# Kernel optimization log

Hardware: AMD Instinct MI355X
Metric: run time of the kernel (lower is better)

## Reference

```python
import jax, jax.numpy as jnp
import numpy as np

EPS = 1e-8
HIDDEN = 200


def _dsmall(n, d):
    # torch: d = d*(d>eps) + eps*(d<=eps); n/d
    return n / jnp.where(d > EPS, d, EPS)


def _mp_match(v1, v2, w):
    # v1: (B,S,H); v2: (B,S,H) or (B,H); w: (L,H) -> (B,S,L)
    wt = w.T[None, None]                      # (1,1,H,L)
    a = v1[..., None] * wt                    # (B,S,H,L)
    if v2.ndim == 2:
        v2 = jnp.broadcast_to(v2[:, None, :], v1.shape)
    b = v2[..., None] * wt                    # (B,S,H,L)
    dot = jnp.sum(a * b, axis=2)
    na = jnp.linalg.norm(a, axis=2)
    nb = jnp.linalg.norm(b, axis=2)
    return dot / jnp.maximum(na * nb, EPS)    # cosine_similarity over H


def _mp_pairwise(v1, v2, w):
    # v1: (B,S1,H); v2: (B,S2,H); w: (L,H) -> (B,S1,S2,L)
    a = v1[:, None] * w[None, :, None]        # (B,L,S1,H)
    b = v2[:, None] * w[None, :, None]        # (B,L,S2,H)
    na = jnp.linalg.norm(a, axis=3, keepdims=True)   # (B,L,S1,1)
    nb = jnp.linalg.norm(b, axis=3, keepdims=True)   # (B,L,S2,1)
    n = jnp.einsum('blph,blqh->blpq', a, b)
    d = na * jnp.swapaxes(nb, 2, 3)
    return jnp.transpose(_dsmall(n, d), (0, 2, 3, 1))


def _attention(v1, v2):
    # cosine-similarity matrix (B,S1,S2)
    n1 = jnp.linalg.norm(v1, axis=2, keepdims=True)           # (B,S1,1)
    n2 = jnp.linalg.norm(v2, axis=2, keepdims=True)           # (B,S2,1)
    a = jnp.einsum('bph,bqh->bpq', v1, v2)
    return _dsmall(a, n1 * jnp.swapaxes(n2, 1, 2))


def _matching(con_p, con_h, w1, w2, w3, w4, w5, w6, w7, w8):
    p_fw, p_bw = con_p[..., :HIDDEN], con_p[..., HIDDEN:]
    h_fw, h_bw = con_h[..., :HIDDEN], con_h[..., HIDDEN:]

    # 1) full matching
    mv_p_full_fw = _mp_match(p_fw, h_fw[:, -1, :], w1)
    mv_p_full_bw = _mp_match(p_bw, h_bw[:, 0, :], w2)
    mv_h_full_fw = _mp_match(h_fw, p_fw[:, -1, :], w1)
    mv_h_full_bw = _mp_match(h_bw, p_bw[:, 0, :], w2)

    # 2) maxpooling matching
    mv_max_fw = _mp_pairwise(p_fw, h_fw, w3)  # (B,S1,S2,L)
    mv_max_bw = _mp_pairwise(p_bw, h_bw, w4)
    mv_p_max_fw = jnp.max(mv_max_fw, axis=2)
    mv_p_max_bw = jnp.max(mv_max_bw, axis=2)
    mv_h_max_fw = jnp.max(mv_max_fw, axis=1)
    mv_h_max_bw = jnp.max(mv_max_bw, axis=1)

    # 3) attentive matching (mean)
    att_fw = _attention(p_fw, h_fw)           # (B,S1,S2)
    att_bw = _attention(p_bw, h_bw)

    # sum of att_h over dim 2 is a matmul (same math, no (B,S1,S2,H) tensor)
    att_h_sum_fw = jnp.einsum('bpq,bqh->bph', att_fw, h_fw)
    att_h_sum_bw = jnp.einsum('bpq,bqh->bph', att_bw, h_bw)
    att_p_sum_fw = jnp.einsum('bpq,bph->bqh', att_fw, p_fw)
    att_p_sum_bw = jnp.einsum('bpq,bph->bqh', att_bw, p_bw)

    att_mean_h_fw = _dsmall(att_h_sum_fw, jnp.sum(att_fw, axis=2, keepdims=True))
    att_mean_h_bw = _dsmall(att_h_sum_bw, jnp.sum(att_bw, axis=2, keepdims=True))
    att_mean_p_fw = _dsmall(att_p_sum_fw, jnp.swapaxes(jnp.sum(att_fw, axis=1, keepdims=True), 1, 2))
    att_mean_p_bw = _dsmall(att_p_sum_bw, jnp.swapaxes(jnp.sum(att_bw, axis=1, keepdims=True), 1, 2))

    mv_p_att_mean_fw = _mp_match(p_fw, att_mean_h_fw, w5)
    mv_p_att_mean_bw = _mp_match(p_bw, att_mean_h_bw, w6)
    mv_h_att_mean_fw = _mp_match(h_fw, att_mean_p_fw, w5)
    mv_h_att_mean_bw = _mp_match(h_bw, att_mean_p_bw, w6)

    # 4) max-attentive matching (needs full (B,S1,S2,H) broadcast for the max)
    att_h_fw = h_fw[:, None, :, :] * att_fw[:, :, :, None]   # (B,S1,S2,H)
    att_h_bw = h_bw[:, None, :, :] * att_bw[:, :, :, None]
    att_p_fw = p_fw[:, :, None, :] * att_fw[:, :, :, None]
    att_p_bw = p_bw[:, :, None, :] * att_bw[:, :, :, None]

    att_max_h_fw = jnp.max(att_h_fw, axis=2)                 # (B,S1,H)
    att_max_h_bw = jnp.max(att_h_bw, axis=2)
    att_max_p_fw = jnp.max(att_p_fw, axis=1)                 # (B,S2,H)
    att_max_p_bw = jnp.max(att_p_bw, axis=1)

    mv_p_att_max_fw = _mp_match(p_fw, att_max_h_fw, w7)
    mv_p_att_max_bw = _mp_match(p_bw, att_max_h_bw, w8)
    mv_h_att_max_fw = _mp_match(h_fw, att_max_p_fw, w7)
    mv_h_att_max_bw = _mp_match(h_bw, att_max_p_bw, w8)

    mv_p = jnp.concatenate([mv_p_full_fw, mv_p_max_fw, mv_p_att_mean_fw, mv_p_att_max_fw,
                            mv_p_full_bw, mv_p_max_bw, mv_p_att_mean_bw, mv_p_att_max_bw], axis=2)
    mv_h = jnp.concatenate([mv_h_full_fw, mv_h_max_fw, mv_h_att_mean_fw, mv_h_att_max_fw,
                            mv_h_full_bw, mv_h_max_bw, mv_h_att_mean_bw, mv_h_att_max_bw], axis=2)
    # dropout is identity in inference mode
    return mv_p, mv_h


def setup_inputs() -> dict:
    key = jax.random.key(0)
    ks = jax.random.split(key, 10)
    B, S, H, L = 32, 64, HIDDEN, 20
    w_std = np.sqrt(2.0 / H)  # kaiming_normal fan_in
    inp = {
        'con_p': jax.random.normal(ks[0], (B, S, 2 * H), dtype=jnp.float32),
        'con_h': jax.random.normal(ks[1], (B, S, 2 * H), dtype=jnp.float32),
    }
    for i in range(8):
        inp[f'mp_w{i+1}'] = jax.random.normal(ks[2 + i], (L, H), dtype=jnp.float32) * w_std
    return inp


def reference(con_p, con_h, mp_w1, mp_w2, mp_w3, mp_w4, mp_w5, mp_w6, mp_w7, mp_w8):
    return _matching(con_p, con_h, mp_w1, mp_w2, mp_w3, mp_w4, mp_w5, mp_w6, mp_w7, mp_w8)
```

## Files before the change

kernel.cpp:

```cpp
#include <hip/hip_runtime.h>
#include <hip/hip_bf16.h>
#include <math.h>

#define EPS 1e-8f
#define BB 32
#define SS 64
#define HH 200
#define LL 20
#define KST 232
#define S16ST 72
#define BHST 72
#define MLST 208

typedef float f32x4 __attribute__((ext_vector_type(4)));
typedef _Float16 f16x8v __attribute__((ext_vector_type(8)));
typedef _Float16 f16x2 __attribute__((ext_vector_type(2)));

__global__ __launch_bounds__(512, 4) void fused_all_kernel(
        const float* __restrict__ conp, const float* __restrict__ conh,
        const float* __restrict__ w1, const float* __restrict__ w2,
        const float* __restrict__ w3, const float* __restrict__ w4,
        const float* __restrict__ w5, const float* __restrict__ w6,
        const float* __restrict__ w7, const float* __restrict__ w8,
        float* __restrict__ out) {
    __shared__ __align__(16) float smem[19104];
    int t = threadIdx.x;

    int rem, grp;
    if (blockIdx.x < 256) {
        rem = 2;
        grp = ((blockIdx.x & 7) * 32) + (blockIdx.x >> 3);
    } else {
        int abid = blockIdx.x - 256;
        int aidx = ((abid & 7) * 64) + (abid >> 3);
        rem = aidx & 1;
        grp = aidx >> 1;
    }

    if (rem < 2) {
        _Float16* AT16 = (_Float16*)smem;
        _Float16* BT16 = (_Float16*)(smem + 1856);
        _Float16* BHh  = (_Float16*)(smem + 9280);
        _Float16* S16h = (_Float16*)(smem + 16768);
        float* nrmA  = smem + 17344;
        float* nrmB  = smem + 17360;
        _Float16* meanLh = (_Float16*)(smem + 17440);
        _Float16* PB = (_Float16*)smem;
        _Float16* WB = (_Float16*)(smem + 5568);

        int blk = grp * 2 + rem;
        int qh = blk & 3;
        int sdb = blk >> 2;
        int b = sdb & 31, sd = sdb >> 5;
        int dir = sd & 1, side = sd >> 1;
        const float* selfb = side ? conh : conp;
        const float* oppb  = side ? conp : conh;
        int fidx = dir ? 0 : (SS - 1);
        const float* fvr = oppb + (b * SS + fidx) * (2 * HH) + dir * HH;

        int arow = t / 25, ack = t % 25;

        float xr[8], yv0[8];
        if (t < 400) {
            const float* xp = selfb + (b * SS + qh * 16 + arow) * (2 * HH) + dir * HH + ack * 8;
            *(float4*)&xr[0] = *(const float4*)xp; *(float4*)&xr[4] = *(const float4*)(xp + 4);
            *(float4*)&yv0[0] = *(const float4*)(fvr + ack * 8);
            *(float4*)&yv0[4] = *(const float4*)(fvr + ack * 8 + 4);
            f16x8v r8;
#pragma unroll
            for (int i = 0; i < 8; ++i) r8[i] = (_Float16)xr[i];
            *(f16x8v*)&AT16[arow * KST + ack * 8] = r8;
        }
        {
            f16x8v z8 = (f16x8v)(_Float16)0.f;
            if (t < 312) {
                if (t < 48) { int row = t / 3, ckp = 25 + t % 3;
                    *(f16x8v*)&AT16[row * KST + ckp * 8] = z8;
                } else if (t < 240) { int e2 = t - 48; int row = e2 / 3, ckp = 25 + e2 % 3;
                    *(f16x8v*)&BT16[row * KST + ckp * 8] = z8;
                } else { int e2 = t - 240; int row = 200 + e2 / 9, c8 = (e2 % 9) * 8;
                    *(f16x8v*)&BHh[row * BHST + c8] = z8;
                }
            }
        }
        for (int e = t; e < 1600; e += 512) {
            int rw = e / 25, ck = e % 25, k = ck * 8;
            const float* xp = oppb + (b * SS + rw) * (2 * HH) + dir * HH + k;
            float xv[8];
            *(float4*)&xv[0] = *(const float4*)xp; *(float4*)&xv[4] = *(const float4*)(xp + 4);
            f16x8v r8;
#pragma unroll
            for (int i = 0; i < 8; ++i) r8[i] = (_Float16)xv[i];
            *(f16x8v*)&BT16[rw * KST + k] = r8;
        }
        __syncthreads();

        int wv_ = __builtin_amdgcn_readfirstlane(t >> 6);
        int lane = t & 63;
        int q = lane >> 4, c = lane & 15;

        f32x4 accS = (f32x4){0.f, 0.f, 0.f, 0.f};
        if (wv_ < 4) {
            int ct = wv_;
            for (int ks = 0; ks < 7; ++ks) {
                int kb = ks * 32 + q * 8;
                f16x8v af  = *(const f16x8v*)&AT16[c * KST + kb];
                f16x8v bf_ = *(const f16x8v*)&BT16[(ct * 16 + c) * KST + kb];
                accS = __builtin_amdgcn_mfma_f32_16x16x32_f16(af, bf_, accS, 0, 0, 0);
            }
        } else {
            int dt = wv_ - 4;
            f32x4 accB = (f32x4){0.f, 0.f, 0.f, 0.f};
            for (int ks = 0; ks < 7; ++ks) {
                int kb = ks * 32 + q * 8;
                f16x8v bf_ = *(const f16x8v*)&BT16[(dt * 16 + c) * KST + kb];
                accB = __builtin_amdgcn_mfma_f32_16x16x32_f16(bf_, bf_, accB, 0, 0, 0);
            }
            if ((c >> 2) == q) nrmB[dt * 16 + c] = accB[c & 3];
            if (dt == 0) {
                f32x4 accA = (f32x4){0.f, 0.f, 0.f, 0.f};
                for (int ks = 0; ks < 7; ++ks) {
                    int kb = ks * 32 + q * 8;
                    f16x8v af = *(const f16x8v*)&AT16[c * KST + kb];
                    accA = __builtin_amdgcn_mfma_f32_16x16x32_f16(af, af, accA, 0, 0, 0);
                }
                if ((c >> 2) == q) nrmA[c] = accA[c & 3];
            } else {
                for (int ch = dt - 1; ch < 25; ch += 3) {
                    f16x8v v = *(const f16x8v*)&BT16[lane * KST + ch * 8];
#pragma unroll
                    for (int i = 0; i < 8; ++i) BHh[(ch * 8 + i) * BHST + lane] = v[i];
                }
            }
        }
        __syncthreads();

        if (wv_ < 4) {
            int col = wv_ * 16 + c;
            float no = sqrtf(nrmB[col]);
#pragma unroll
            for (int r = 0; r < 4; ++r) {
                int row = q * 4 + r;
                float ns = sqrtf(nrmA[row]);
                S16h[row * S16ST + col] = (_Float16)(accS[r] / fmaxf(ns * no, EPS));
            }
        }
        __syncthreads();

        float wf0[8], wf1[8], wf2[8];
        if (t < 500) {
            int wl = t / 25, wck = t % 25;
            const float* wp0 = (dir ? w2 : w1) + wl * HH + wck * 8;
            const float* wp1 = (dir ? w6 : w5) + wl * HH + wck * 8;
            const float* wp2 = (dir ? w8 : w7) + wl * HH + wck * 8;
            *(float4*)&wf0[0] = *(const float4*)wp0; *(float4*)&wf0[4] = *(const float4*)(wp0 + 4);
            *(float4*)&wf1[0] = *(const float4*)wp1; *(float4*)&wf1[4] = *(const float4*)(wp1 + 4);
            *(float4*)&wf2[0] = *(const float4*)wp2; *(float4*)&wf2[4] = *(const float4*)(wp2 + 4);
        }

        f16x2 mx0, mx1, mx2, mx3;
        {
            f16x2 ninf = {(_Float16)(-INFINITY), (_Float16)(-INFINITY)};
            mx0 = ninf; mx1 = ninf; mx2 = ninf; mx3 = ninf;
        }
        if (wv_ == 7) {
            for (int nt = 0; nt < 13; ++nt) {
                f32x4 macc = (f32x4){0.f, 0.f, 0.f, 0.f};
#pragma unroll
                for (int k2 = 0; k2 < 2; ++k2) {
                    int kb = k2 * 32 + q * 8;
                    f16x8v sa = *(const f16x8v*)&S16h[c * S16ST + kb];
                    f16x8v bh = *(const f16x8v*)&BHh[(nt * 16 + c) * BHST + kb];
                    macc = __builtin_amdgcn_mfma_f32_16x16x32_f16(sa, bh, macc, 0, 0, 0);
                }
                int h = nt * 16 + c;
                if (h < 200) {
#pragma unroll
                    for (int r = 0; r < 4; ++r)
                        meanLh[(q * 4 + r) * MLST + h] = (_Float16)(macc[r] * 0.125f);
                }
            }
        } else if (t < 400) {
            const _Float16* srow = &S16h[arow * S16ST];
            const _Float16* bcol = &BT16[ack * 8];
            for (int kg = 0; kg < 8; ++kg) {
                f16x8v sr = *(const f16x8v*)&srow[kg * 8];
#pragma unroll
                for (int kk = 0; kk < 8; ++kk) {
                    _Float16 sh = sr[kk];
                    f16x2 sv = {sh, sh};
                    f16x8v bv = *(const f16x8v*)&bcol[(kg * 8 + kk) * KST];
                    f16x2 p0 = sv * __builtin_shufflevector(bv, bv, 0, 1);
                    f16x2 p1 = sv * __builtin_shufflevector(bv, bv, 2, 3);
                    f16x2 p2 = sv * __builtin_shufflevector(bv, bv, 4, 5);
                    f16x2 p3 = sv * __builtin_shufflevector(bv, bv, 6, 7);
                    mx0 = __builtin_elementwise_max(mx0, p0);
                    mx1 = __builtin_elementwise_max(mx1, p1);
                    mx2 = __builtin_elementwise_max(mx2, p2);
                    mx3 = __builtin_elementwise_max(mx3, p3);
                }
            }
        }
        __syncthreads();

#pragma unroll
        for (int m = 0; m < 3; ++m) {
            if (t < 400) {
                float yv[8];
                if (m == 0) {
#pragma unroll
                    for (int i = 0; i < 8; ++i) yv[i] = yv0[i];
                } else if (m == 1) {
                    f16x8v yl = *(const f16x8v*)&meanLh[arow * MLST + ack * 8];
#pragma unroll
                    for (int i = 0; i < 8; ++i) yv[i] = (float)yl[i];
                } else {
                    yv[0] = (float)mx0[0]; yv[1] = (float)mx0[1];
                    yv[2] = (float)mx1[0]; yv[3] = (float)mx1[1];
                    yv[4] = (float)mx2[0]; yv[5] = (float)mx2[1];
                    yv[6] = (float)mx3[0]; yv[7] = (float)mx3[1];
                }
                f16x8v r1, r2;
#pragma unroll
                for (int i = 0; i < 8; ++i) {
                    r1[i] = (_Float16)(xr[i] * yv[i]);
                    r2[i] = (_Float16)(yv[i] * yv[i]);
                }
                if (m == 0) {
                    f16x8v r0;
#pragma unroll
                    for (int i = 0; i < 8; ++i) r0[i] = (_Float16)(xr[i] * xr[i]);
                    *(f16x8v*)&PB[(0 * 16 + arow) * KST + ack * 8] = r0;
                }
                *(f16x8v*)&PB[(1 * 16 + arow) * KST + ack * 8] = r1;
                *(f16x8v*)&PB[(2 * 16 + arow) * KST + ack * 8] = r2;
            }
            if (t < 500) {
                int wl = t / 25, wck = t % 25;
                f16x8v wr;
                if (m == 0) {
#pragma unroll
                    for (int i = 0; i < 8; ++i) wr[i] = (_Float16)(wf0[i] * wf0[i]);
                } else if (m == 1) {
#pragma unroll
                    for (int i = 0; i < 8; ++i) wr[i] = (_Float16)(wf1[i] * wf1[i]);
                } else {
#pragma unroll
                    for (int i = 0; i < 8; ++i) wr[i] = (_Float16)(wf2[i] * wf2[i]);
                }
                *(f16x8v*)&WB[wl * KST + wck * 8] = wr;
            }
            if (m == 0) {
                f16x8v z8 = (f16x8v)(_Float16)0.f;
                for (int e = t; e < 540; e += 512) {
                    if (e < 144) { int row = e / 3, ckp = 25 + e % 3;
                        *(f16x8v*)&PB[row * KST + ckp * 8] = z8;
                    } else if (e < 480) { int e2 = e - 144; int row = 20 + e2 / 28, ckp = e2 % 28;
                        *(f16x8v*)&WB[row * KST + ckp * 8] = z8;
                    } else { int e2 = e - 480; int row = e2 / 3, ckp = 25 + e2 % 3;
                        *(f16x8v*)&WB[row * KST + ckp * 8] = z8;
                    }
                }
            }
            __syncthreads();

            if (wv_ < 2) {
                int ntile = wv_;
                f32x4 accA = (f32x4){0.f, 0.f, 0.f, 0.f};
                f32x4 accD = (f32x4){0.f, 0.f, 0.f, 0.f};
                f32x4 accB = (f32x4){0.f, 0.f, 0.f, 0.f};
                for (int ks = 0; ks < 7; ++ks) {
                    int kb = ks * 32 + q * 8;
                    f16x8v bfw = *(const f16x8v*)&WB[(ntile * 16 + c) * KST + kb];
                    f16x8v a0 = *(const f16x8v*)&PB[(0 * 16 + c) * KST + kb];
                    f16x8v a1 = *(const f16x8v*)&PB[(1 * 16 + c) * KST + kb];
                    f16x8v a2 = *(const f16x8v*)&PB[(2 * 16 + c) * KST + kb];
                    accA = __builtin_amdgcn_mfma_f32_16x16x32_f16(a0, bfw, accA, 0, 0, 0);
                    accD = __builtin_amdgcn_mfma_f32_16x16x32_f16(a1, bfw, accD, 0, 0, 0);
                    accB = __builtin_amdgcn_mfma_f32_16x16x32_f16(a2, bfw, accB, 0, 0, 0);
                }
                int l_ = ntile * 16 + c;
                if (l_ < LL) {
                    int chunk = (m == 0) ? 0 : (m == 1) ? 40 : 60;
#pragma unroll
                    for (int r = 0; r < 4; ++r) {
                        int s = qh * 16 + q * 4 + r;
                        float cosv = accD[r] / fmaxf(sqrtf(accA[r] * accB[r]), EPS);
                        out[side * (BB * SS * 160) + (b * SS + s) * 160 + dir * 80 + chunk + l_] = cosv;
                    }
                }
            }
            if (m < 2) __syncthreads();
        }
    } else {
        _Float16* ATr = (_Float16*)smem;
        _Float16* BTr = (_Float16*)(smem + 7424);
        _Float16* w2L = (_Float16*)(smem + 14848);
        float* nA5  = smem + 15432;
        float* nB5  = smem + 15752;
        float* cmL5 = smem + 16072;

        int cblk = grp;
        int lg = cblk & 3;
        int db = cblk >> 2;
        int b = db & 31, dir = db >> 5;
        int l0 = lg * 5;
        const float* wsrc = dir ? w4 : w3;
        const float* Ag = conp + dir * HH;
        const float* Bg = conh + dir * HH;

        for (int e = t; e < 3200; e += 512) {
            int half = (e >= 1600) ? 1 : 0;
            int e2 = e - half * 1600;
            int rw = e2 / 25, ck = e2 % 25, k = ck * 8;
            const float* xp = (half ? Bg : Ag) + (b * SS + rw) * (2 * HH) + k;
            float xv[8];
            *(float4*)&xv[0] = *(const float4*)xp; *(float4*)&xv[4] = *(const float4*)(xp + 4);
            f16x8v r8;
#pragma unroll
            for (int i = 0; i < 8; ++i) r8[i] = (_Float16)xv[i];
            _Float16* dst = half ? BTr : ATr;
            *(f16x8v*)&dst[rw * KST + k] = r8;
        }
        {
            f16x8v z8 = (f16x8v)(_Float16)0.f;
            if (t < 384) {
                int half = (t >= 192) ? 1 : 0;
                int e2 = t - half * 192;
                int row = e2 / 3, ckp = 25 + e2 % 3;
                _Float16* dst = half ? BTr : ATr;
                *(f16x8v*)&dst[row * KST + ckp * 8] = z8;
            } else if (t < 399) {
                int e2 = t - 384;
                int wl = e2 / 3, ckp = 25 + e2 % 3;
                *(f16x8v*)&w2L[wl * KST + ckp * 8] = z8;
            }
            if (t < 125) {
                int wl = t / 25, wck = t % 25;
                const float* wp = wsrc + (l0 + wl) * HH + wck * 8;
                float wvv[8];
                *(float4*)&wvv[0] = *(const float4*)wp; *(float4*)&wvv[4] = *(const float4*)(wp + 4);
                f16x8v r8;
#pragma unroll
                for (int i = 0; i < 8; ++i) r8[i] = (_Float16)(wvv[i] * wvv[i]);
                *(f16x8v*)&w2L[wl * KST + wck * 8] = r8;
            }
        }
        __syncthreads();

        int wv_ = __builtin_amdgcn_readfirstlane(t >> 6);
        int lane = t & 63;
        int q = lane >> 4, c = lane & 15;
        int m0 = (wv_ & 3) * 16;

        f32x4 z4 = (f32x4){0.f, 0.f, 0.f, 0.f};
        f32x4 acc0[4] = {z4, z4, z4, z4};
        f32x4 acc1[4] = {z4, z4, z4, z4};
        f32x4 acc2[4] = {z4, z4, z4, z4};

        if (wv_ < 4) {
            for (int ks = 0; ks < 7; ++ks) {
                int kb = ks * 32 + q * 8;
                f16x8v ar  = *(const f16x8v*)&ATr[(m0 + c) * KST + kb];
                f16x8v ww0 = *(const f16x8v*)&w2L[0 * KST + kb];
                f16x8v ww1 = *(const f16x8v*)&w2L[1 * KST + kb];
                f16x8v ww2 = *(const f16x8v*)&w2L[2 * KST + kb];
                f16x8v af0 = ar * ww0, af1 = ar * ww1, af2 = ar * ww2;
#pragma unroll
                for (int ct = 0; ct < 4; ++ct) {
                    f16x8v br = *(const f16x8v*)&BTr[(ct * 16 + c) * KST + kb];
                    acc0[ct] = __builtin_amdgcn_mfma_f32_16x16x32_f16(af0, br, acc0[ct], 0, 0, 0);
                    acc1[ct] = __builtin_amdgcn_mfma_f32_16x16x32_f16(af1, br, acc1[ct], 0, 0, 0);
                    acc2[ct] = __builtin_amdgcn_mfma_f32_16x16x32_f16(af2, br, acc2[ct], 0, 0, 0);
                }
            }
        } else {
            int d0 = (wv_ - 4) * 16;
            f32x4 nacA[5] = {z4, z4, z4, z4, z4};
            f32x4 nacB[5] = {z4, z4, z4, z4, z4};
            for (int ks = 0; ks < 7; ++ks) {
                int kb = ks * 32 + q * 8;
                f16x8v ar = *(const f16x8v*)&ATr[(d0 + c) * KST + kb];
                f16x8v br = *(const f16x8v*)&BTr[(d0 + c) * KST + kb];
#pragma unroll
                for (int li = 0; li < 5; ++li) {
                    f16x8v wf = *(const f16x8v*)&w2L[li * KST + kb];
                    f16x8v afw = ar * wf;
                    f16x8v bfw = br * wf;
                    nacA[li] = __builtin_amdgcn_mfma_f32_16x16x32_f16(afw, ar, nacA[li], 0, 0, 0);
                    nacB[li] = __builtin_amdgcn_mfma_f32_16x16x32_f16(bfw, br, nacB[li], 0, 0, 0);
                }
            }
            if ((c >> 2) == q) {
#pragma unroll
                for (int li = 0; li < 5; ++li) {
                    nA5[li * 64 + d0 + c] = nacA[li][c & 3];
                    nB5[li * 64 + d0 + c] = nacB[li][c & 3];
                }
            }
        }
        __syncthreads();

#define C_EPI(LI, ACC) do { \
    float na_[4], nb_[4]; \
    _Pragma("unroll") for (int r_ = 0; r_ < 4; ++r_) na_[r_] = sqrtf(nA5[(LI) * 64 + m0 + q * 4 + r_]); \
    _Pragma("unroll") for (int ct_ = 0; ct_ < 4; ++ct_) nb_[ct_] = sqrtf(nB5[(LI) * 64 + ct_ * 16 + c]); \
    float rowm_[4] = {-INFINITY, -INFINITY, -INFINITY, -INFINITY}; \
    float colm_[4] = {-INFINITY, -INFINITY, -INFINITY, -INFINITY}; \
    _Pragma("unroll") for (int ct_ = 0; ct_ < 4; ++ct_) { \
        _Pragma("unroll") for (int r_ = 0; r_ < 4; ++r_) { \
            float cv_ = (ACC)[ct_][r_] / fmaxf(na_[r_] * nb_[ct_], EPS); \
            rowm_[r_] = fmaxf(rowm_[r_], cv_); \
            colm_[ct_] = fmaxf(colm_[ct_], cv_); \
        } \
    } \
    _Pragma("unroll") for (int r_ = 0; r_ < 4; ++r_) { \
        float v_ = rowm_[r_]; \
        v_ = fmaxf(v_, __shfl_xor(v_, 1, 64)); \
        v_ = fmaxf(v_, __shfl_xor(v_, 2, 64)); \
        v_ = fmaxf(v_, __shfl_xor(v_, 4, 64)); \
        v_ = fmaxf(v_, __shfl_xor(v_, 8, 64)); \
        rowm_[r_] = v_; \
    } \
    if (c == 0) { \
        _Pragma("unroll") for (int r_ = 0; r_ < 4; ++r_) \
            out[(b * SS + m0 + q * 4 + r_) * 160 + dir * 80 + 20 + l0 + (LI)] = rowm_[r_]; \
    } \
    _Pragma("unroll") for (int ct_ = 0; ct_ < 4; ++ct_) { \
        float v_ = colm_[ct_]; \
        v_ = fmaxf(v_, __shfl_xor(v_, 16, 64)); \
        v_ = fmaxf(v_, __shfl_xor(v_, 32, 64)); \
        colm_[ct_] = v_; \
    } \
    if (q == 0) { \
        _Pragma("unroll") for (int ct_ = 0; ct_ < 4; ++ct_) \
            cmL5[(LI) * 256 + wv_ * 64 + ct_ * 16 + c] = colm_[ct_]; \
    } \
} while (0)

        if (wv_ < 4) {
            C_EPI(0, acc0);
            C_EPI(1, acc1);
            C_EPI(2, acc2);
            f32x4 acc3[4] = {z4, z4, z4, z4};
            f32x4 acc4[4] = {z4, z4, z4, z4};
            for (int ks = 0; ks < 7; ++ks) {
                int kb = ks * 32 + q * 8;
                f16x8v ar  = *(const f16x8v*)&ATr[(m0 + c) * KST + kb];
                f16x8v ww3 = *(const f16x8v*)&w2L[3 * KST + kb];
                f16x8v ww4 = *(const f16x8v*)&w2L[4 * KST + kb];
                f16x8v af3 = ar * ww3, af4 = ar * ww4;
#pragma unroll
                for (int ct = 0; ct < 4; ++ct) {
                    f16x8v br = *(const f16x8v*)&BTr[(ct * 16 + c) * KST + kb];
                    acc3[ct] = __builtin_amdgcn_mfma_f32_16x16x32_f16(af3, br, acc3[ct], 0, 0, 0);
                    acc4[ct] = __builtin_amdgcn_mfma_f32_16x16x32_f16(af4, br, acc4[ct], 0, 0, 0);
                }
            }
            C_EPI(3, acc3);
            C_EPI(4, acc4);
        }
        __syncthreads();

        if (t < 320) {
            int li = t >> 6, j = t & 63;
            const float* cm = &cmL5[li * 256];
            float mm = fmaxf(fmaxf(cm[j], cm[64 + j]), fmaxf(cm[128 + j], cm[192 + j]));
            out[BB * SS * 160 + (b * SS + j) * 160 + dir * 80 + 20 + l0 + li] = mm;
        }
#undef C_EPI
    }
}

extern "C" void kernel_launch(void* const* d_in, const int* in_sizes, int n_in,
                              void* d_out, int out_size, void* d_ws, size_t ws_size,
                              hipStream_t stream) {
    const float* conp = (const float*)d_in[0];
    const float* conh = (const float*)d_in[1];
    const float* w1 = (const float*)d_in[2];
    const float* w2 = (const float*)d_in[3];
    const float* w3 = (const float*)d_in[4];
    const float* w4 = (const float*)d_in[5];
    const float* w5 = (const float*)d_in[6];
    const float* w6 = (const float*)d_in[7];
    const float* w7 = (const float*)d_in[8];
    const float* w8 = (const float*)d_in[9];
    float* out = (float*)d_out;
    (void)d_ws; (void)ws_size;

    fused_all_kernel<<<768, 512, 0, stream>>>(conp, conh,
                                              w1, w2, w3, w4, w5, w6, w7, w8, out);
}
```

Measured before the change: 99.67 us.

## Double-buffer PB/WB staging to overlap MFMA with next stage in matching blocks

Adds a second pair of LDS staging buffers so that staging the operands for the next matching stage overlaps the MFMA cosine computation of the current stage. This removes one barrier per stage. Shared memory per block grows to about 80 KB, which may limit how many blocks fit per CU. The x*x row is now recomputed and stored in every stage, since both buffers need it.

```diff
diff --git a/kernel.cpp b/kernel.cpp
--- a/kernel.cpp
+++ b/kernel.cpp
@@ -23,7 +23,7 @@
         const float* __restrict__ w5, const float* __restrict__ w6,
         const float* __restrict__ w7, const float* __restrict__ w8,
         float* __restrict__ out) {
-    __shared__ __align__(16) float smem[19104];
+    __shared__ __align__(16) float smem[20224];
     int t = threadIdx.x;
 
     int rem, grp;
@@ -44,9 +44,11 @@
         _Float16* S16h = (_Float16*)(smem + 16768);
         float* nrmA  = smem + 17344;
         float* nrmB  = smem + 17360;
-        _Float16* meanLh = (_Float16*)(smem + 17440);
-        _Float16* PB = (_Float16*)smem;
-        _Float16* WB = (_Float16*)(smem + 5568);
+        _Float16* meanLh = (_Float16*)(smem + 18560);
+        _Float16* PB0 = (_Float16*)smem;
+        _Float16* WB0 = (_Float16*)(smem + 5568);
+        _Float16* PB1 = (_Float16*)(smem + 9280);
+        _Float16* WB1 = (_Float16*)(smem + 14848);
 
         int blk = grp * 2 + rem;
         int qh = blk & 3;
@@ -203,95 +205,98 @@
         }
         __syncthreads();
 
-#pragma unroll
-        for (int m = 0; m < 3; ++m) {
-            if (t < 400) {
-                float yv[8];
-                if (m == 0) {
-#pragma unroll
-                    for (int i = 0; i < 8; ++i) yv[i] = yv0[i];
-                } else if (m == 1) {
-                    f16x8v yl = *(const f16x8v*)&meanLh[arow * MLST + ack * 8];
-#pragma unroll
-                    for (int i = 0; i < 8; ++i) yv[i] = (float)yl[i];
-                } else {
-                    yv[0] = (float)mx0[0]; yv[1] = (float)mx0[1];
-                    yv[2] = (float)mx1[0]; yv[3] = (float)mx1[1];
-                    yv[4] = (float)mx2[0]; yv[5] = (float)mx2[1];
-                    yv[6] = (float)mx3[0]; yv[7] = (float)mx3[1];
-                }
-                f16x8v r1, r2;
-#pragma unroll
-                for (int i = 0; i < 8; ++i) {
-                    r1[i] = (_Float16)(xr[i] * yv[i]);
-                    r2[i] = (_Float16)(yv[i] * yv[i]);
-                }
-                if (m == 0) {
-                    f16x8v r0;
-#pragma unroll
-                    for (int i = 0; i < 8; ++i) r0[i] = (_Float16)(xr[i] * xr[i]);
-                    *(f16x8v*)&PB[(0 * 16 + arow) * KST + ack * 8] = r0;
-                }
-                *(f16x8v*)&PB[(1 * 16 + arow) * KST + ack * 8] = r1;
-                *(f16x8v*)&PB[(2 * 16 + arow) * KST + ack * 8] = r2;
-            }
-            if (t < 500) {
-                int wl = t / 25, wck = t % 25;
-                f16x8v wr;
-                if (m == 0) {
-#pragma unroll
-                    for (int i = 0; i < 8; ++i) wr[i] = (_Float16)(wf0[i] * wf0[i]);
-                } else if (m == 1) {
-#pragma unroll
-                    for (int i = 0; i < 8; ++i) wr[i] = (_Float16)(wf1[i] * wf1[i]);
-                } else {
-#pragma unroll
-                    for (int i = 0; i < 8; ++i) wr[i] = (_Float16)(wf2[i] * wf2[i]);
-                }
-                *(f16x8v*)&WB[wl * KST + wck * 8] = wr;
-            }
-            if (m == 0) {
-                f16x8v z8 = (f16x8v)(_Float16)0.f;
-                for (int e = t; e < 540; e += 512) {
-                    if (e < 144) { int row = e / 3, ckp = 25 + e % 3;
-                        *(f16x8v*)&PB[row * KST + ckp * 8] = z8;
-                    } else if (e < 480) { int e2 = e - 144; int row = 20 + e2 / 28, ckp = e2 % 28;
-                        *(f16x8v*)&WB[row * KST + ckp * 8] = z8;
-                    } else { int e2 = e - 480; int row = e2 / 3, ckp = 25 + e2 % 3;
-                        *(f16x8v*)&WB[row * KST + ckp * 8] = z8;
-                    }
-                }
-            }
-            __syncthreads();
-
-            if (wv_ < 2) {
-                int ntile = wv_;
-                f32x4 accA = (f32x4){0.f, 0.f, 0.f, 0.f};
-                f32x4 accD = (f32x4){0.f, 0.f, 0.f, 0.f};
-                f32x4 accB = (f32x4){0.f, 0.f, 0.f, 0.f};
-                for (int ks = 0; ks < 7; ++ks) {
-                    int kb = ks * 32 + q * 8;
-                    f16x8v bfw = *(const f16x8v*)&WB[(ntile * 16 + c) * KST + kb];
-                    f16x8v a0 = *(const f16x8v*)&PB[(0 * 16 + c) * KST + kb];
-                    f16x8v a1 = *(const f16x8v*)&PB[(1 * 16 + c) * KST + kb];
-                    f16x8v a2 = *(const f16x8v*)&PB[(2 * 16 + c) * KST + kb];
-                    accA = __builtin_amdgcn_mfma_f32_16x16x32_f16(a0, bfw, accA, 0, 0, 0);
-                    accD = __builtin_amdgcn_mfma_f32_16x16x32_f16(a1, bfw, accD, 0, 0, 0);
-                    accB = __builtin_amdgcn_mfma_f32_16x16x32_f16(a2, bfw, accB, 0, 0, 0);
-                }
-                int l_ = ntile * 16 + c;
-                if (l_ < LL) {
-                    int chunk = (m == 0) ? 0 : (m == 1) ? 40 : 60;
-#pragma unroll
-                    for (int r = 0; r < 4; ++r) {
-                        int s = qh * 16 + q * 4 + r;
-                        float cosv = accD[r] / fmaxf(sqrtf(accA[r] * accB[r]), EPS);
-                        out[side * (BB * SS * 160) + (b * SS + s) * 160 + dir * 80 + chunk + l_] = cosv;
-                    }
-                }
-            }
-            if (m < 2) __syncthreads();
-        }
+#define STAGE_M(MM, PBd, WBd) do { \
+    if (t < 400) { \
+        float yv[8]; \
+        if ((MM) == 0) { \
+            _Pragma("unroll") for (int i = 0; i < 8; ++i) yv[i] = yv0[i]; \
+        } else if ((MM) == 1) { \
+            f16x8v yl = *(const f16x8v*)&meanLh[arow * MLST + ack * 8]; \
+            _Pragma("unroll") for (int i = 0; i < 8; ++i) yv[i] = (float)yl[i]; \
+        } else { \
+            yv[0] = (float)mx0[0]; yv[1] = (float)mx0[1]; \
+            yv[2] = (float)mx1[0]; yv[3] = (float)mx1[1]; \
+            yv[4] = (float)mx2[0]; yv[5] = (float)mx2[1]; \
+            yv[6] = (float)mx3[0]; yv[7] = (float)mx3[1]; \
+        } \
+        f16x8v r0, r1, r2; \
+        _Pragma("unroll") for (int i = 0; i < 8; ++i) { \
+            r0[i] = (_Float16)(xr[i] * xr[i]); \
+            r1[i] = (_Float16)(xr[i] * yv[i]); \
+            r2[i] = (_Float16)(yv[i] * yv[i]); \
+        } \
+        *(f16x8v*)&(PBd)[(0 * 16 + arow) * KST + ack * 8] = r0; \
+        *(f16x8v*)&(PBd)[(1 * 16 + arow) * KST + ack * 8] = r1; \
+        *(f16x8v*)&(PBd)[(2 * 16 + arow) * KST + ack * 8] = r2; \
+    } \
+    if (t < 500) { \
+        int wl_ = t / 25, wck_ = t % 25; \
+        f16x8v wr; \
+        if ((MM) == 0) { _Pragma("unroll") for (int i = 0; i < 8; ++i) wr[i] = (_Float16)(wf0[i] * wf0[i]); } \
+        else if ((MM) == 1) { _Pragma("unroll") for (int i = 0; i < 8; ++i) wr[i] = (_Float16)(wf1[i] * wf1[i]); } \
+        else { _Pragma("unroll") for (int i = 0; i < 8; ++i) wr[i] = (_Float16)(wf2[i] * wf2[i]); } \
+        *(f16x8v*)&(WBd)[wl_ * KST + wck_ * 8] = wr; \
+    } \
+} while (0)
+
+#define MFMA_M(MM, PBd, WBd) do { \
+    if (wv_ < 2) { \
+        int ntile = wv_; \
+        f32x4 accA = (f32x4){0.f, 0.f, 0.f, 0.f}; \
+        f32x4 accD = (f32x4){0.f, 0.f, 0.f, 0.f}; \
+        f32x4 accB = (f32x4){0.f, 0.f, 0.f, 0.f}; \
+        for (int ks = 0; ks < 7; ++ks) { \
+            int kb = ks * 32 + q * 8; \
+            f16x8v bfw = *(const f16x8v*)&(WBd)[(ntile * 16 + c) * KST + kb]; \
+            f16x8v a0 = *(const f16x8v*)&(PBd)[(0 * 16 + c) * KST + kb]; \
+            f16x8v a1 = *(const f16x8v*)&(PBd)[(1 * 16 + c) * KST + kb]; \
+            f16x8v a2 = *(const f16x8v*)&(PBd)[(2 * 16 + c) * KST + kb]; \
+            accA = __builtin_amdgcn_mfma_f32_16x16x32_f16(a0, bfw, accA, 0, 0, 0); \
+            accD = __builtin_amdgcn_mfma_f32_16x16x32_f16(a1, bfw, accD, 0, 0, 0); \
+            accB = __builtin_amdgcn_mfma_f32_16x16x32_f16(a2, bfw, accB, 0, 0, 0); \
+        } \
+        int l_ = ntile * 16 + c; \
+        if (l_ < LL) { \
+            int chunk = ((MM) == 0) ? 0 : ((MM) == 1) ? 40 : 60; \
+            _Pragma("unroll") for (int r = 0; r < 4; ++r) { \
+                int s = qh * 16 + q * 4 + r; \
+                float cosv = accD[r] / fmaxf(sqrtf(accA[r] * accB[r]), EPS); \
+                out[side * (BB * SS * 160) + (b * SS + s) * 160 + dir * 80 + chunk + l_] = cosv; \
+            } \
+        } \
+    } \
+} while (0)
+
+        STAGE_M(0, PB0, WB0);
+        {
+            f16x8v z8 = (f16x8v)(_Float16)0.f;
+            for (int e = t; e < 1080; e += 512) {
+                int bsel = (e >= 540);
+                int e2 = e - bsel * 540;
+                _Float16* PBd = bsel ? PB1 : PB0;
+                _Float16* WBd = bsel ? WB1 : WB0;
+                if (e2 < 144) { int row = e2 / 3, ckp = 25 + e2 % 3;
+                    *(f16x8v*)&PBd[row * KST + ckp * 8] = z8;
+                } else if (e2 < 480) { int e3 = e2 - 144; int row = 20 + e3 / 28, ckp = e3 % 28;
+                    *(f16x8v*)&WBd[row * KST + ckp * 8] = z8;
+                } else { int e3 = e2 - 480; int row = e3 / 3, ckp = 25 + e3 % 3;
+                    *(f16x8v*)&WBd[row * KST + ckp * 8] = z8;
+                }
+            }
+        }
+        __syncthreads();
+
+        MFMA_M(0, PB0, WB0);
+        STAGE_M(1, PB1, WB1);
+        __syncthreads();
+
+        MFMA_M(1, PB1, WB1);
+        STAGE_M(2, PB0, WB0);
+        __syncthreads();
+
+        MFMA_M(2, PB0, WB0);
+#undef STAGE_M
+#undef MFMA_M
     } else {
         _Float16* ATr = (_Float16*)smem;
         _Float16* BTr = (_Float16*)(smem + 7424);
```

After: 99.00 us. Within noise of the previous version (-0.7%).
